# Performance work log

Hardware: AMD Instinct MI355X
Metric: run time of the kernel (lower is better)

Reference implementation:

```python
import jax, jax.numpy as jnp
import numpy as np

N = 20000      # nodes
L = 64         # seq_length
E = 64         # emb_size
V = 30000      # vocab_size
HG = 128       # gnn_hidden_size
HT = 128       # text_hidden_size
NE = 640000    # edges
EPS = 1e-12


def _normalize(x):
    # F.normalize(x, p=2, dim=1) on [N, E, L]
    n = jnp.sqrt(jnp.sum(x * x, axis=1, keepdims=True))
    return x / jnp.maximum(n, EPS)


def gcn_conv(x, W, b, src_idx, dst_idx, n_nodes):
    # PyG GCNConv: add self-loops, symmetric normalization D^-1/2 (A+I) D^-1/2 (X W) + b
    h = x @ W                                            # [N, out]
    deg = jnp.zeros((n_nodes,), h.dtype).at[dst_idx].add(1.0) + 1.0  # incl. self-loop
    dinv = jax.lax.rsqrt(deg)
    norm = dinv[src_idx] * dinv[dst_idx]                 # [NE]
    msg = h[src_idx] * norm[:, None]                     # gather + scale
    out = jnp.zeros_like(h).at[dst_idx].add(msg)         # scatter-add to targets
    out = out + h * (dinv * dinv)[:, None]               # self-loop term
    return out + b


def setup_inputs() -> dict:
    key = jax.random.key(0)
    ks = jax.random.split(key, 12)
    rn = lambda k, shape: jax.random.normal(k, shape, jnp.float32) * 0.02
    return {
        "src": jax.random.randint(ks[0], (N, L), 0, V),
        "seg": jax.random.randint(ks[1], (N, L), 0, 3),
        "edge_index": jax.random.randint(ks[2], (2, NE), 0, N),
        "src_emb": rn(ks[3], (V, E)),
        "seg_emb": rn(ks[4], (3, E)),
        "w": jnp.ones((L,), jnp.float32),
        "Wq1": rn(ks[5], (E, HT)), "bq1": jnp.zeros((HT,), jnp.float32),
        "Wq2": rn(ks[6], (HT, E)), "bq2": jnp.zeros((E,), jnp.float32),
        "Wg1": rn(ks[7], (E, HG)), "bg1": jnp.zeros((HG,), jnp.float32),
        "Wg2": rn(ks[8], (HG, E)), "bg2": jnp.zeros((E,), jnp.float32),
        "Wl": rn(ks[9], (E, E)),   "bl": jnp.zeros((E,), jnp.float32),
    }


def reference(src, seg, edge_index, src_emb, seg_emb, w, Wq1, bq1, Wq2, bq2,
              Wg1, bg1, Wg2, bg2, Wl, bl):
    # --- LiteratureEmbedding ---
    se = src_emb[src]                 # [N, L, E]
    ge = seg_emb[seg]                 # [N, L, E]
    sv = se.reshape(-1, E, L)         # raw view (matches torch .view, not transpose)
    gv = ge.reshape(-1, E, L)
    f = (_normalize(w * sv) + _normalize(gv)).sum(-1)   # [N, E]
    # --- query MLP ---
    x = jax.nn.relu(f @ Wq1 + bq1) @ Wq2 + bq2
    # --- two GCN layers ---
    si, di = edge_index[0], edge_index[1]
    x = jax.nn.relu(gcn_conv(x, Wg1, bg1, si, di, N))
    x = jax.nn.relu(gcn_conv(x, Wg2, bg2, si, di, N))
    # --- output linear (dropout is identity in eval) ---
    return x @ Wl + bl
```

## Files before the change

### kernel.cpp

```cpp
#include <hip/hip_runtime.h>

#if defined(__has_builtin)
#if __has_builtin(__builtin_amdgcn_readlane)
#define READLANE(v, l) __builtin_amdgcn_readlane((v), (l))
#else
#define READLANE(v, l) __shfl((v), (l))
#endif
#else
#define READLANE(v, l) __shfl((v), (l))
#endif
__device__ __forceinline__ float readlane_f(float v, int l) {
    return __uint_as_float(READLANE(__float_as_uint(v), l));
}

#define CAPLOG 8

__global__ __launch_bounds__(256) void zero_cursor_k(int* __restrict__ p, int n) {
    int i = blockIdx.x * 256 + threadIdx.x;
    if (i < n) p[i] = 0;
}

__global__ __launch_bounds__(256) void fillb_k(const int* __restrict__ si,
                                               const int* __restrict__ di,
                                               int* __restrict__ cursor,
                                               int* __restrict__ edge_off, int ne) {
    int i = blockIdx.x * 256 + threadIdx.x;
    if (i < ne) {
        int d = di[i];
        int pos = atomicAdd(cursor + d, 1);
        edge_off[((long)d << CAPLOG) + pos] = si[i] << 8;
    }
}

__global__ __launch_bounds__(256) void dinv_k(const int* __restrict__ deg,
                                              float* __restrict__ dinv, int n) {
    int i = blockIdx.x * 256 + threadIdx.x;
    if (i < n) dinv[i] = rsqrtf((float)deg[i] + 1.0f);
}

__device__ __forceinline__ float csr_gather(const char* __restrict__ hb,
                                            const int* __restrict__ eo,
                                            int dn, int j, int j4, float acc)
{
#define LDV(mm) (*(const float*)(hb + (READLANE(eoff, m + mm) + j4)))
    for (int e = 0; e < dn; e += 64) {
        const int cnt = min(dn - e, 64);
        const int eoff = (e + j < dn) ? eo[e + j] : 0;
        int m = 0;
        float a0 = 0.f, a1 = 0.f, a2 = 0.f, a3 = 0.f;
        for (; m + 16 <= cnt; m += 16) {
            float v0 = LDV(0),  v1 = LDV(1),  v2 = LDV(2),  v3 = LDV(3);
            float v4 = LDV(4),  v5 = LDV(5),  v6 = LDV(6),  v7 = LDV(7);
            float v8 = LDV(8),  v9 = LDV(9),  v10 = LDV(10), v11 = LDV(11);
            float v12 = LDV(12), v13 = LDV(13), v14 = LDV(14), v15 = LDV(15);
            a0 += (v0 + v1) + (v2 + v3);
            a1 += (v4 + v5) + (v6 + v7);
            a2 += (v8 + v9) + (v10 + v11);
            a3 += (v12 + v13) + (v14 + v15);
        }
        for (; m + 4 <= cnt; m += 4) {
            float v0 = LDV(0), v1 = LDV(1), v2 = LDV(2), v3 = LDV(3);
            a0 += (v0 + v1) + (v2 + v3);
        }
        for (; m < cnt; ++m) a0 += LDV(0);
        acc += (a0 + a1) + (a2 + a3);
    }
#undef LDV
    return acc;
}

__global__ __launch_bounds__(256) void embed_k(
    const int* __restrict__ src, const int* __restrict__ seg,
    const float* __restrict__ src_emb, const float* __restrict__ seg_emb,
    const float* __restrict__ wvec, float* __restrict__ f)
{
    __shared__ __align__(16) float S[64 * 65];
    __shared__ float red[4][64];
    __shared__ float part2[4][64];
    __shared__ float coef[64];
    __shared__ float rGs[64];
    __shared__ float segE[192];
    __shared__ float dG[3];
    __shared__ int   gidxS[64];
    __shared__ int   cnt3[3];

    const int t = threadIdx.x, wid = t >> 6, q = t & 63;
    const long n = blockIdx.x;

    if (wid == 0) {
        int c = seg[n * 64 + q];
        gidxS[q] = c;
        unsigned long long b0 = __ballot(c == 0);
        unsigned long long b1 = __ballot(c == 1);
        if (q == 0) {
            int n0 = __popcll(b0), n1 = __popcll(b1);
            cnt3[0] = n0; cnt3[1] = n1; cnt3[2] = 64 - n0 - n1;
        }
    } else if (t < 64 + 192) {
        segE[t - 64] = seg_emb[t - 64];
    }

    const int p0 = wid * 16;
    int off = src[n * 64 + p0 + (q & 15)] << 8;
    const char* base = (const char*)src_emb;
    const int q4 = q << 2;
    float s2 = 0.f;
    #pragma unroll
    for (int pp = 0; pp < 16; ++pp) {
        int so = READLANE(off, pp);
        float v = *(const float*)(base + (so + q4));
        S[(p0 + pp) * 65 + q] = v;
        s2 += v * v;
    }
    red[wid][q] = s2;
    __syncthreads();

    if (t < 64) {
        float ts = red[0][t] + red[1][t] + red[2][t] + red[3][t];
        float wq = wvec[t];
        coef[t] = wq / fmaxf(fabsf(wq) * sqrtf(ts), 1e-12f);
        float e0 = segE[t], e1 = segE[64 + t], e2 = segE[128 + t];
        float g2 = (float)cnt3[0] * e0 * e0 + (float)cnt3[1] * e1 * e1
                 + (float)cnt3[2] * e2 * e2;
        rGs[t] = 1.f / fmaxf(sqrtf(g2), 1e-12f);
    }
    __syncthreads();

    if (t < 3) {
        float a = 0.f;
        for (int k = 0; k < 64; ++k) a += segE[t * 64 + k] * rGs[k];
        dG[t] = a;
    }
    float acc = 0.f;
    const int k0 = wid * 16;
    #pragma unroll
    for (int kk = 0; kk < 16; ++kk)
        acc += S[q * 65 + k0 + kk] * coef[k0 + kk];
    part2[wid][q] = acc;
    __syncthreads();

    if (t < 64)
        f[n * 64 + t] = part2[0][t] + part2[1][t] + part2[2][t] + part2[3][t]
                        + dG[gidxS[t]];
}

template <bool S2_BIAS>
__device__ __forceinline__ void dense_pair_body(
    float* Wbuf, float* F, float* H,
    const float* __restrict__ b1, const float* __restrict__ W2,
    const float* __restrict__ b2, const float* __restrict__ rs,
    float* __restrict__ out, int row0, int nrows, int t)
{
    {
        const int jg = t & 31, rslot = t >> 5;
        const int j0 = jg * 4;
        float4 acc[2];
        float4 b4 = *(const float4*)&b1[j0];
        acc[0] = b4; acc[1] = b4;
        #pragma unroll 2
        for (int k = 0; k < 64; k += 4) {
            float4 w0 = *(float4*)&Wbuf[(k + 0) * 128 + j0];
            float4 w1 = *(float4*)&Wbuf[(k + 1) * 128 + j0];
            float4 w2 = *(float4*)&Wbuf[(k + 2) * 128 + j0];
            float4 w3 = *(float4*)&Wbuf[(k + 3) * 128 + j0];
            #pragma unroll
            for (int i = 0; i < 2; ++i) {
                float4 fq = *(float4*)&F[(rslot + i * 8) * 64 + k];
                acc[i].x += fq.x * w0.x + fq.y * w1.x + fq.z * w2.x + fq.w * w3.x;
                acc[i].y += fq.x * w0.y + fq.y * w1.y + fq.z * w2.y + fq.w * w3.y;
                acc[i].z += fq.x * w0.z + fq.y * w1.z + fq.z * w2.z + fq.w * w3.z;
                acc[i].w += fq.x * w0.w + fq.y * w1.w + fq.z * w2.w + fq.w * w3.w;
            }
        }
        #pragma unroll
        for (int i = 0; i < 2; ++i) {
            float4 v;
            v.x = fmaxf(acc[i].x, 0.f); v.y = fmaxf(acc[i].y, 0.f);
            v.z = fmaxf(acc[i].z, 0.f); v.w = fmaxf(acc[i].w, 0.f);
            *(float4*)&H[(rslot + i * 8) * 128 + j0] = v;
        }
    }
    __syncthreads();

    for (int i = t * 4; i < 128 * 64; i += 1024)
        *(float4*)&Wbuf[i] = *(const float4*)&W2[i];
    __syncthreads();

    {
        const int jg2 = t & 15, r2 = t >> 4;
        const int j0 = jg2 * 4;
        float4 acc = S2_BIAS ? *(const float4*)&b2[j0]
                             : make_float4(0.f, 0.f, 0.f, 0.f);
        #pragma unroll 2
        for (int k = 0; k < 128; k += 4) {
            float4 w0 = *(float4*)&Wbuf[(k + 0) * 64 + j0];
            float4 w1 = *(float4*)&Wbuf[(k + 1) * 64 + j0];
            float4 w2 = *(float4*)&Wbuf[(k + 2) * 64 + j0];
            float4 w3 = *(float4*)&Wbuf[(k + 3) * 64 + j0];
            float4 fq = *(float4*)&H[r2 * 128 + k];
            acc.x += fq.x * w0.x + fq.y * w1.x + fq.z * w2.x + fq.w * w3.x;
            acc.y += fq.x * w0.y + fq.y * w1.y + fq.z * w2.y + fq.w * w3.y;
            acc.z += fq.x * w0.z + fq.y * w1.z + fq.z * w2.z + fq.w * w3.z;
            acc.w += fq.x * w0.w + fq.y * w1.w + fq.z * w2.w + fq.w * w3.w;
        }
        const int r = row0 + r2;
        if (r < nrows) {
            float sc = rs[r];
            float4 v;
            v.x = acc.x * sc; v.y = acc.y * sc; v.z = acc.z * sc; v.w = acc.w * sc;
            *(float4*)&out[(long)r * 64 + j0] = v;
        }
    }
}

template <bool S2_BIAS>
__global__ __launch_bounds__(256, 4) void fused2_k(
    const float* __restrict__ in, const float* __restrict__ W1,
    const float* __restrict__ b1, const float* __restrict__ W2,
    const float* __restrict__ b2, const float* __restrict__ rs,
    float* __restrict__ out, int nrows)
{
    __shared__ __align__(16) float Wbuf[64 * 128];
    __shared__ __align__(16) float F[16 * 64];
    __shared__ __align__(16) float H[16 * 128];
    const int t = threadIdx.x;
    const int row0 = blockIdx.x * 16;

    for (int i = t * 4; i < 64 * 128; i += 1024)
        *(float4*)&Wbuf[i] = *(const float4*)&W1[i];
    for (int i = t * 4; i < 16 * 64; i += 1024) {
        int r = i >> 6;
        float4 v = make_float4(0.f, 0.f, 0.f, 0.f);
        if (row0 + r < nrows) v = *(const float4*)&in[(long)row0 * 64 + i];
        *(float4*)&F[i] = v;
    }
    __syncthreads();
    dense_pair_body<S2_BIAS>(Wbuf, F, H, b1, W2, b2, rs, out, row0, nrows, t);
}

__global__ __launch_bounds__(256, 4) void gcnfused_k(
    const float* __restrict__ C, const int* __restrict__ deg,
    const int* __restrict__ edge_off, const float* __restrict__ dinv,
    const float* __restrict__ W1, const float* __restrict__ b1,
    const float* __restrict__ W2, float* __restrict__ out, int nrows)
{
    __shared__ __align__(16) float Wbuf[64 * 128];
    __shared__ __align__(16) float F[16 * 64];
    __shared__ __align__(16) float H[16 * 128];
    const int t = threadIdx.x;
    const int row0 = blockIdx.x * 16;
    const int wv = t >> 6, j = t & 63;

    for (int i = t * 4; i < 64 * 128; i += 1024)
        *(float4*)&Wbuf[i] = *(const float4*)&W1[i];

    const char* hb = (const char*)C;
    const int j4 = j << 2;
    #pragma unroll
    for (int i = 0; i < 4; ++i) {
        const int r = wv * 4 + i;
        const int node = row0 + r;
        float res = 0.f;
        if (node < nrows) {
            float acc = csr_gather(hb, edge_off + ((long)node << CAPLOG),
                                   deg[node], j, j4, C[(long)node * 64 + j]);
            res = dinv[node] * acc;
        }
        F[r * 64 + j] = res;
    }
    __syncthreads();
    dense_pair_body<false>(Wbuf, F, H, b1, W2, nullptr, dinv, out, row0, nrows, t);
}

__global__ __launch_bounds__(256) void gatherout_k(
    const float* __restrict__ hp, const int* __restrict__ deg,
    const int* __restrict__ edge_off, const float* __restrict__ dinv,
    const float* __restrict__ bg2, const float* __restrict__ Wl,
    const float* __restrict__ bl, float* __restrict__ out, int n)
{
    __shared__ __align__(16) float WlL[64 * 64];
    const int t = threadIdx.x;
    for (int i = t * 4; i < 64 * 64; i += 1024)
        *(float4*)&WlL[i] = *(const float4*)&Wl[i];
    __syncthreads();

    const int row0 = blockIdx.x * 16;
    const int wv = t >> 6, j = t & 63;
    const char* hb = (const char*)hp;
    const int j4 = j << 2;
    const float bgj = bg2[j];
    const float blj = bl[j];

    #pragma unroll
    for (int i = 0; i < 4; ++i) {
        const int node = row0 + wv * 4 + i;
        if (node >= n) continue;
        float acc = csr_gather(hb, edge_off + ((long)node << CAPLOG),
                               deg[node], j, j4, hp[(long)node * 64 + j]);
        const float v = fmaxf(dinv[node] * acc + bgj, 0.f);

        float o = blj;
        #pragma unroll 4
        for (int k = 0; k < 64; k += 4) {
            float vk0 = readlane_f(v, k + 0);
            float vk1 = readlane_f(v, k + 1);
            float vk2 = readlane_f(v, k + 2);
            float vk3 = readlane_f(v, k + 3);
            o += vk0 * WlL[(k + 0) * 64 + j] + vk1 * WlL[(k + 1) * 64 + j]
               + vk2 * WlL[(k + 2) * 64 + j] + vk3 * WlL[(k + 3) * 64 + j];
        }
        out[(long)node * 64 + j] = o;
    }
}

extern "C" void kernel_launch(void* const* d_in, const int* in_sizes, int n_in,
                              void* d_out, int out_size, void* d_ws, size_t ws_size,
                              hipStream_t stream) {
    const int*   src     = (const int*)  d_in[0];
    const int*   seg     = (const int*)  d_in[1];
    const int*   ei      = (const int*)  d_in[2];
    const float* src_emb = (const float*)d_in[3];
    const float* seg_emb = (const float*)d_in[4];
    const float* w       = (const float*)d_in[5];
    const float* Wq1     = (const float*)d_in[6];
    const float* bq1     = (const float*)d_in[7];
    const float* Wq2     = (const float*)d_in[8];
    const float* bq2     = (const float*)d_in[9];
    const float* Wg1     = (const float*)d_in[10];
    const float* bg1     = (const float*)d_in[11];
    const float* Wg2     = (const float*)d_in[12];
    const float* bg2     = (const float*)d_in[13];
    const float* Wl      = (const float*)d_in[14];
    const float* bl      = (const float*)d_in[15];
    float* out = (float*)d_out;

    const int N  = in_sizes[0] / 64;
    const int NE = in_sizes[2] / 2;
    const int* si = ei;
    const int* di = ei + NE;

    const size_t Npad = ((size_t)N + 3) & ~(size_t)3;
    int*   cursor   = (int*)d_ws;
    int*   edge_off = cursor + Npad;
    float* dinv     = (float*)(edge_off + ((size_t)N << CAPLOG));
    float* A = dinv + Npad;
    float* C = A + (size_t)N * 64;

    dim3 b256(256);
    const int nBlocks = (N + 255) / 256;
    const int eBlocks = (NE + 255) / 256;
    const int fBlocks = (N + 15) / 16;

    zero_cursor_k<<<nBlocks, b256, 0, stream>>>(cursor, N);
    fillb_k      <<<eBlocks, b256, 0, stream>>>(si, di, cursor, edge_off, NE);
    dinv_k       <<<nBlocks, b256, 0, stream>>>(cursor, dinv, N);

    embed_k<<<N, b256, 0, stream>>>(src, seg, src_emb, seg_emb, w, A);

    fused2_k<true><<<fBlocks, b256, 0, stream>>>(A, Wq1, bq1, Wq2, bq2, dinv, C, N);

    gcnfused_k<<<fBlocks, b256, 0, stream>>>(C, cursor, edge_off, dinv,
                                             Wg1, bg1, Wg2, A, N);

    gatherout_k<<<fBlocks, b256, 0, stream>>>(A, cursor, edge_off, dinv, bg2,
                                              Wl, bl, out, N);
}
```

Before: 256.7 us.

## Vectorize CSR gather with float4 loads across four edges per wavefront

The neighbor gather is restructured so each wavefront splits into four groups of 16 lanes. Each lane loads a float4 of a neighbor row, so four edges are fetched per instruction instead of one scalar load per lane per edge, and the partial sums are combined with cross-lane shuffles. Out-of-range slots point at a zeroed padding row appended after each feature buffer, which dinv_k now clears. This cuts the number of load instructions and readlane operations in the memory-bound gather, at the cost of extra shuffle reductions and a workspace layout change.

```diff
diff --git a/kernel.cpp b/kernel.cpp
--- a/kernel.cpp
+++ b/kernel.cpp
@@ -33,40 +33,55 @@
 }
 
 __global__ __launch_bounds__(256) void dinv_k(const int* __restrict__ deg,
-                                              float* __restrict__ dinv, int n) {
+                                              float* __restrict__ dinv,
+                                              float* __restrict__ Azero,
+                                              float* __restrict__ Czero, int n) {
     int i = blockIdx.x * 256 + threadIdx.x;
     if (i < n) dinv[i] = rsqrtf((float)deg[i] + 1.0f);
-}
-
-__device__ __forceinline__ float csr_gather(const char* __restrict__ hb,
-                                            const int* __restrict__ eo,
-                                            int dn, int j, int j4, float acc)
-{
-#define LDV(mm) (*(const float*)(hb + (READLANE(eoff, m + mm) + j4)))
+    if (i < 64) { Azero[i] = 0.f; Czero[i] = 0.f; }
+}
+
+__device__ __forceinline__ float4 csr_gather4(const char* __restrict__ hb,
+                                              const int* __restrict__ eo,
+                                              int dn, int j, int zoff)
+{
+    const int grp = j >> 4;
+    const int col = (j & 15) << 4;
+    float4 a0 = make_float4(0.f, 0.f, 0.f, 0.f);
+    float4 a1 = a0, a2 = a0, a3 = a0;
     for (int e = 0; e < dn; e += 64) {
         const int cnt = min(dn - e, 64);
-        const int eoff = (e + j < dn) ? eo[e + j] : 0;
+        const int eoff = (e + j < dn) ? eo[e + j] : zoff;
         int m = 0;
-        float a0 = 0.f, a1 = 0.f, a2 = 0.f, a3 = 0.f;
         for (; m + 16 <= cnt; m += 16) {
-            float v0 = LDV(0),  v1 = LDV(1),  v2 = LDV(2),  v3 = LDV(3);
-            float v4 = LDV(4),  v5 = LDV(5),  v6 = LDV(6),  v7 = LDV(7);
-            float v8 = LDV(8),  v9 = LDV(9),  v10 = LDV(10), v11 = LDV(11);
-            float v12 = LDV(12), v13 = LDV(13), v14 = LDV(14), v15 = LDV(15);
-            a0 += (v0 + v1) + (v2 + v3);
-            a1 += (v4 + v5) + (v6 + v7);
-            a2 += (v8 + v9) + (v10 + v11);
-            a3 += (v12 + v13) + (v14 + v15);
-        }
-        for (; m + 4 <= cnt; m += 4) {
-            float v0 = LDV(0), v1 = LDV(1), v2 = LDV(2), v3 = LDV(3);
-            a0 += (v0 + v1) + (v2 + v3);
-        }
-        for (; m < cnt; ++m) a0 += LDV(0);
-        acc += (a0 + a1) + (a2 + a3);
-    }
-#undef LDV
-    return acc;
+            int o0 = __shfl(eoff, m + grp);
+            int o1 = __shfl(eoff, m + 4 + grp);
+            int o2 = __shfl(eoff, m + 8 + grp);
+            int o3 = __shfl(eoff, m + 12 + grp);
+            float4 v0 = *(const float4*)(hb + (o0 + col));
+            float4 v1 = *(const float4*)(hb + (o1 + col));
+            float4 v2 = *(const float4*)(hb + (o2 + col));
+            float4 v3 = *(const float4*)(hb + (o3 + col));
+            a0.x += v0.x; a0.y += v0.y; a0.z += v0.z; a0.w += v0.w;
+            a1.x += v1.x; a1.y += v1.y; a1.z += v1.z; a1.w += v1.w;
+            a2.x += v2.x; a2.y += v2.y; a2.z += v2.z; a2.w += v2.w;
+            a3.x += v3.x; a3.y += v3.y; a3.z += v3.z; a3.w += v3.w;
+        }
+        for (; m < cnt; m += 4) {
+            int o = __shfl(eoff, m + grp);
+            float4 v = *(const float4*)(hb + (o + col));
+            a0.x += v.x; a0.y += v.y; a0.z += v.z; a0.w += v.w;
+        }
+    }
+    a0.x += a1.x + a2.x + a3.x;
+    a0.y += a1.y + a2.y + a3.y;
+    a0.z += a1.z + a2.z + a3.z;
+    a0.w += a1.w + a2.w + a3.w;
+    a0.x += __shfl_xor(a0.x, 16); a0.x += __shfl_xor(a0.x, 32);
+    a0.y += __shfl_xor(a0.y, 16); a0.y += __shfl_xor(a0.y, 32);
+    a0.z += __shfl_xor(a0.z, 16); a0.z += __shfl_xor(a0.z, 32);
+    a0.w += __shfl_xor(a0.w, 16); a0.w += __shfl_xor(a0.w, 32);
+    return a0;
 }
 
 __global__ __launch_bounds__(256) void embed_k(
@@ -242,7 +257,7 @@
     const float* __restrict__ C, const int* __restrict__ deg,
     const int* __restrict__ edge_off, const float* __restrict__ dinv,
     const float* __restrict__ W1, const float* __restrict__ b1,
-    const float* __restrict__ W2, float* __restrict__ out, int nrows)
+    const float* __restrict__ W2, float* __restrict__ out, int nrows, int zoff)
 {
     __shared__ __align__(16) float Wbuf[64 * 128];
     __shared__ __align__(16) float F[16 * 64];
@@ -250,23 +265,32 @@
     const int t = threadIdx.x;
     const int row0 = blockIdx.x * 16;
     const int wv = t >> 6, j = t & 63;
+    const int col = (j & 15) << 4;
 
     for (int i = t * 4; i < 64 * 128; i += 1024)
         *(float4*)&Wbuf[i] = *(const float4*)&W1[i];
 
     const char* hb = (const char*)C;
-    const int j4 = j << 2;
     #pragma unroll
     for (int i = 0; i < 4; ++i) {
         const int r = wv * 4 + i;
         const int node = row0 + r;
-        float res = 0.f;
         if (node < nrows) {
-            float acc = csr_gather(hb, edge_off + ((long)node << CAPLOG),
-                                   deg[node], j, j4, C[(long)node * 64 + j]);
-            res = dinv[node] * acc;
-        }
-        F[r * 64 + j] = res;
+            float4 agg = csr_gather4(hb, edge_off + ((long)node << CAPLOG),
+                                     deg[node], j, zoff);
+            float4 self = *(const float4*)(hb + ((long)node << 8) + col);
+            float dv = dinv[node];
+            if ((j >> 4) == 0) {
+                float4 res;
+                res.x = dv * (self.x + agg.x);
+                res.y = dv * (self.y + agg.y);
+                res.z = dv * (self.z + agg.z);
+                res.w = dv * (self.w + agg.w);
+                *(float4*)&F[r * 64 + (j & 15) * 4] = res;
+            }
+        } else if ((j >> 4) == 0) {
+            *(float4*)&F[r * 64 + (j & 15) * 4] = make_float4(0.f, 0.f, 0.f, 0.f);
+        }
     }
     __syncthreads();
     dense_pair_body<false>(Wbuf, F, H, b1, W2, nullptr, dinv, out, row0, nrows, t);
@@ -276,9 +300,10 @@
     const float* __restrict__ hp, const int* __restrict__ deg,
     const int* __restrict__ edge_off, const float* __restrict__ dinv,
     const float* __restrict__ bg2, const float* __restrict__ Wl,
-    const float* __restrict__ bl, float* __restrict__ out, int n)
+    const float* __restrict__ bl, float* __restrict__ out, int n, int zoff)
 {
     __shared__ __align__(16) float WlL[64 * 64];
+    __shared__ __align__(16) float vS[4][64];
     const int t = threadIdx.x;
     for (int i = t * 4; i < 64 * 64; i += 1024)
         *(float4*)&WlL[i] = *(const float4*)&Wl[i];
@@ -286,18 +311,26 @@
 
     const int row0 = blockIdx.x * 16;
     const int wv = t >> 6, j = t & 63;
+    const int col = (j & 15) << 4;
     const char* hb = (const char*)hp;
-    const int j4 = j << 2;
-    const float bgj = bg2[j];
     const float blj = bl[j];
+    const float4 bg4 = *(const float4*)&bg2[(j & 15) * 4];
 
     #pragma unroll
     for (int i = 0; i < 4; ++i) {
         const int node = row0 + wv * 4 + i;
         if (node >= n) continue;
-        float acc = csr_gather(hb, edge_off + ((long)node << CAPLOG),
-                               deg[node], j, j4, hp[(long)node * 64 + j]);
-        const float v = fmaxf(dinv[node] * acc + bgj, 0.f);
+        float4 agg = csr_gather4(hb, edge_off + ((long)node << CAPLOG),
+                                 deg[node], j, zoff);
+        float4 self = *(const float4*)(hb + ((long)node << 8) + col);
+        const float dv = dinv[node];
+        float4 vf;
+        vf.x = fmaxf(dv * (self.x + agg.x) + bg4.x, 0.f);
+        vf.y = fmaxf(dv * (self.y + agg.y) + bg4.y, 0.f);
+        vf.z = fmaxf(dv * (self.z + agg.z) + bg4.z, 0.f);
+        vf.w = fmaxf(dv * (self.w + agg.w) + bg4.w, 0.f);
+        if ((j >> 4) == 0) *(float4*)&vS[wv][(j & 15) * 4] = vf;
+        const float v = vS[wv][j];
 
         float o = blj;
         #pragma unroll 4
@@ -344,7 +377,8 @@
     int*   edge_off = cursor + Npad;
     float* dinv     = (float*)(edge_off + ((size_t)N << CAPLOG));
     float* A = dinv + Npad;
-    float* C = A + (size_t)N * 64;
+    float* C = A + (size_t)N * 64 + 64;
+    const int zoff = N << 8;
 
     dim3 b256(256);
     const int nBlocks = (N + 255) / 256;
@@ -353,15 +387,16 @@
 
     zero_cursor_k<<<nBlocks, b256, 0, stream>>>(cursor, N);
     fillb_k      <<<eBlocks, b256, 0, stream>>>(si, di, cursor, edge_off, NE);
-    dinv_k       <<<nBlocks, b256, 0, stream>>>(cursor, dinv, N);
+    dinv_k       <<<nBlocks, b256, 0, stream>>>(cursor, dinv, A + (size_t)N * 64,
+                                                C + (size_t)N * 64, N);
 
     embed_k<<<N, b256, 0, stream>>>(src, seg, src_emb, seg_emb, w, A);
 
     fused2_k<true><<<fBlocks, b256, 0, stream>>>(A, Wq1, bq1, Wq2, bq2, dinv, C, N);
 
     gcnfused_k<<<fBlocks, b256, 0, stream>>>(C, cursor, edge_off, dinv,
-                                             Wg1, bg1, Wg2, A, N);
+                                             Wg1, bg1, Wg2, A, N, zoff);
 
     gatherout_k<<<fBlocks, b256, 0, stream>>>(A, cursor, edge_off, dinv, bg2,
-                                              Wl, bl, out, N);
-}
+                                              Wl, bl, out, N, zoff);
+}
```

Measured after the change: 252.1 us. No clear change (-1.8%).
